# Kernel optimization log

Measured on AMD Instinct MI355X. Metric: run time of the kernel, lower is better.

## Reference

```python
import jax, jax.numpy as jnp
import numpy as np

K = 5
B = 3.0
MIN_BW = 1e-3
MIN_BH = 1e-3
MIN_D = 1e-3


def _mlp(x, w0, b0, w1, b1):
    # Linear -> Tanh -> Linear (hidden_dim=[512])
    return jnp.tanh(x @ w0 + b0) @ w1 + b1


def _unconstrained_rqs(x, Wu, Hu, Du):
    """Rational-quadratic spline (forward), identity outside [-B, B].
    x: [N, D2]; Wu/Hu: [N, D2, K]; Du: [N, D2, K-1].
    Note: faithful to the torch code, Wu/Hu arrive already softmaxed*2B and Du
    already softplused in NSF_CL.forward, then RQS re-normalizes them again."""
    inside = (x >= -B) & (x <= B)
    const = float(np.log(np.exp(1.0 - MIN_D) - 1.0))
    Dp = jnp.pad(Du, ((0, 0), (0, 0), (1, 1)), constant_values=const)  # [N,D2,K+1]

    widths = jax.nn.softmax(Wu, axis=-1)
    widths = MIN_BW + (1.0 - MIN_BW * K) * widths
    cw = jnp.pad(jnp.cumsum(widths, axis=-1), ((0, 0), (0, 0), (1, 0)))
    cw = 2.0 * B * cw - B
    cw = cw.at[..., 0].set(-B).at[..., -1].set(B)
    widths = cw[..., 1:] - cw[..., :-1]

    heights = jax.nn.softmax(Hu, axis=-1)
    heights = MIN_BH + (1.0 - MIN_BH * K) * heights
    ch = jnp.pad(jnp.cumsum(heights, axis=-1), ((0, 0), (0, 0), (1, 0)))
    ch = 2.0 * B * ch - B
    ch = ch.at[..., 0].set(-B).at[..., -1].set(B)
    heights = ch[..., 1:] - ch[..., :-1]

    deriv = MIN_D + jax.nn.softplus(Dp)  # [N,D2,K+1]

    xc = jnp.clip(x, -B, B)
    # bin search: index of bin containing xc
    idx = jnp.clip(jnp.sum((xc[..., None] >= cw).astype(jnp.int32), axis=-1) - 1, 0, K - 1)
    idx1 = idx[..., None]

    def g(a):
        return jnp.take_along_axis(a, idx1, axis=-1)[..., 0]

    in_cw = g(cw)
    in_w = g(widths)
    in_ch = g(ch)
    in_h = g(heights)
    delta = g(heights / widths)
    d_k = g(deriv)
    d_k1 = jnp.take_along_axis(deriv, idx1 + 1, axis=-1)[..., 0]

    theta = (xc - in_cw) / in_w
    t1m = theta * (1.0 - theta)
    numerator = in_h * (delta * theta * theta + d_k * t1m)
    denominator = delta + (d_k + d_k1 - 2.0 * delta) * t1m
    y = in_ch + numerator / denominator

    deriv_num = delta * delta * (d_k1 * theta * theta + 2.0 * delta * t1m + d_k * (1.0 - theta) ** 2)
    ld = jnp.log(deriv_num) - 2.0 * jnp.log(denominator)
    return jnp.where(inside, y, x), jnp.where(inside, ld, 0.0)


def _cond(out_flat, d2):
    out = out_flat.reshape(-1, d2, 3 * K - 1)
    Wu, Hu, Du = out[..., :K], out[..., K:2 * K], out[..., 2 * K:]
    Wu = 2.0 * B * jax.nn.softmax(Wu, axis=-1)
    Hu = 2.0 * B * jax.nn.softmax(Hu, axis=-1)
    Du = jax.nn.softplus(Du)
    return Wu, Hu, Du


def setup_inputs() -> dict:
    key = jax.random.key(0)
    ks = jax.random.split(key, 5)
    N, dim, hid = 32768, 256, 512
    half = dim // 2
    out_dim = half * (3 * K - 1)
    s0 = 1.0 / np.sqrt(half)
    s1 = 1.0 / np.sqrt(hid)
    return {
        "x": jax.random.normal(ks[0], (N, dim), dtype=jnp.float32),
        "f0_w0": jax.random.normal(ks[1], (half, hid), dtype=jnp.float32) * s0,
        "f0_b0": jnp.zeros((hid,), jnp.float32),
        "f0_w1": jax.random.normal(ks[2], (hid, out_dim), dtype=jnp.float32) * s1,
        "f0_b1": jnp.zeros((out_dim,), jnp.float32),
        "f1_w0": jax.random.normal(ks[3], (half, hid), dtype=jnp.float32) * s0,
        "f1_b0": jnp.zeros((hid,), jnp.float32),
        "f1_w1": jax.random.normal(ks[4], (hid, out_dim), dtype=jnp.float32) * s1,
        "f1_b1": jnp.zeros((out_dim,), jnp.float32),
    }


def reference(x, f0_w0, f0_b0, f0_w1, f0_b1, f1_w0, f1_b0, f1_w1, f1_b1):
    half = x.shape[1] // 2
    x0, x1 = x[:, :half], x[:, half:]
    Wu, Hu, Du = _cond(_mlp(x0, f0_w0, f0_b0, f0_w1, f0_b1), half)
    x1, ld1 = _unconstrained_rqs(x1, Wu, Hu, Du)
    Wu, Hu, Du = _cond(_mlp(x1, f1_w0, f1_b0, f1_w1, f1_b1), half)
    x0, ld0 = _unconstrained_rqs(x0, Wu, Hu, Du)
    z = jnp.concatenate([x0, x1], axis=1)
    log_det = jnp.sum(ld1, axis=1) + jnp.sum(ld0, axis=1)
    return z, log_det
```

## Files before the change

kernel.cpp:

```cpp
#include <hip/hip_runtime.h>
#include <math.h>


#define NROWS 32768
#define DIMX  256
#define HALF  128
#define HID   512
#define BM    64

typedef __attribute__((ext_vector_type(8))) short short8;
typedef __attribute__((ext_vector_type(4))) float f32x4;

__device__ __forceinline__ unsigned short f2bf(float x) {
    unsigned int u = __float_as_uint(x);
    u += 0x7fffu + ((u >> 16) & 1u);
    return (unsigned short)(u >> 16);
}

__device__ __forceinline__ float frcp(float x) { return __builtin_amdgcn_rcpf(x); }

__device__ __forceinline__ float spf(float x) {
    return fmaxf(x, 0.f) + __logf(1.f + __expf(-fabsf(x)));
}

__device__ __forceinline__ void dsm5(const float* P, float* out) {
    float e[5];
    float m = fmaxf(fmaxf(fmaxf(P[0], P[1]), fmaxf(P[2], P[3])), P[4]);
    float s = 0.f;
    #pragma unroll
    for (int p = 0; p < 5; ++p) { e[p] = __expf(P[p] - m); s += e[p]; }
    float r = 6.f * frcp(s);
    float s2 = 0.f;
    #pragma unroll
    for (int p = 0; p < 5; ++p) { e[p] = __expf(e[p] * r); s2 += e[p]; }
    float r2 = 0.995f * frcp(s2);
    #pragma unroll
    for (int p = 0; p < 5; ++p) out[p] = 1.0e-3f + e[p] * r2;
}

__device__ __forceinline__ void rqs_fast(const float* P, float xa, float& yo, float& ldo) {
    float wv[5], hv[5];
    dsm5(P, wv);
    dsm5(P + 5, hv);
    float dvi[4];
    #pragma unroll
    for (int p = 0; p < 4; ++p) dvi[p] = 1.0e-3f + spf(spf(P[10 + p]));
    float xc = fminf(fmaxf(xa, -3.f), 3.f);
    float csw = wv[0], csh = hv[0];
    float in_cw = -3.f, in_ch = -3.f;
    float in_w = 6.f * csw, in_h = 6.f * csh;
    float dk = 1.f, dk1 = dvi[0];
    #pragma unroll
    for (int p = 1; p < 5; ++p) {
        float cwp = 6.f * csw - 3.f;
        float chp = 6.f * csh - 3.f;
        csw += wv[p]; csh += hv[p];
        float cwp1 = (p == 4) ? 3.f : (6.f * csw - 3.f);
        float chp1 = (p == 4) ? 3.f : (6.f * csh - 3.f);
        bool take = (xc >= cwp);
        in_cw = take ? cwp : in_cw;
        in_w  = take ? (cwp1 - cwp) : in_w;
        in_ch = take ? chp : in_ch;
        in_h  = take ? (chp1 - chp) : in_h;
        dk    = take ? dvi[p - 1] : dk;
        dk1   = take ? ((p == 4) ? 1.f : dvi[p]) : dk1;
    }
    float rw = frcp(in_w);
    float th = (xc - in_cw) * rw;
    float om = 1.f - th;
    float t1m = th * om;
    float delta = in_h * rw;
    float num = in_h * (delta * th * th + dk * t1m);
    float den = delta + (dk + dk1 - 2.f * delta) * t1m;
    float y = in_ch + num * frcp(den);
    float dnum = delta * delta * (dk1 * th * th + 2.f * delta * t1m + dk * om * om);
    float ld = __logf(dnum) - 2.f * __logf(den);
    bool inside = (xa >= -3.f) && (xa <= 3.f);
    yo  = inside ? y : xa;
    ldo = inside ? ld : 0.f;
}

__global__ void prep(const float* __restrict__ w1a, const float* __restrict__ w1b,
                     const float* __restrict__ w0a, const float* __restrict__ w0b,
                     const float* __restrict__ b1a, const float* __restrict__ b1b,
                     short* __restrict__ w1f, short* __restrict__ w0f, float* __restrict__ b1p) {
    int idx = blockIdx.x * 256 + threadIdx.x;
    if (idx < 262144) {
        int stage = idx >> 17, rem = idx & 131071;
        int d = rem >> 10, c2 = (rem >> 6) & 15, l = rem & 63;
        const float* src = stage ? w1b : w1a;
        int p = l & 15, g = l >> 4;
        short8 o;
        #pragma unroll
        for (int e = 0; e < 8; ++e) {
            int k = 32 * c2 + 8 * g + e;
            float v = (p < 14) ? src[(size_t)k * 1792 + d * 14 + p] : 0.f;
            o[e] = (short)f2bf(v);
        }
        *reinterpret_cast<short8*>(w1f + (size_t)stage * 1048576 + (size_t)rem * 8) = o;
    } else if (idx < 278528) {
        int r = idx - 262144;
        int stage = r >> 13, rem = r & 8191;
        int l = rem & 63;
        const float* src = stage ? w0b : w0a;
        int p = l & 15, g = l >> 4;
        int ct = rem >> 8, c = (rem >> 6) & 3;
        short8 o;
        #pragma unroll
        for (int e = 0; e < 8; ++e) {
            int k = 32 * c + 8 * g + e;
            o[e] = (short)f2bf(src[k * 512 + ct * 16 + p]);
        }
        *reinterpret_cast<short8*>(w0f + stage * 65536 + rem * 8) = o;
    } else if (idx < 282624) {
        int r = idx - 278528;
        int stage = r >> 11, rem = r & 2047;
        int d = rem >> 4, p = rem & 15;
        const float* src = stage ? b1b : b1a;
        b1p[stage * 2048 + rem] = (p < 14) ? src[d * 14 + p] : 0.f;
    }
}

template <int STAGE>
__global__ __launch_bounds__(256, 2)
void nsf_stage(const float* __restrict__ xin, float* __restrict__ zout,
               float* __restrict__ ld_out,
               const short* __restrict__ w0f, const float* __restrict__ b0,
               const short* __restrict__ w1f, const float* __restrict__ b1p) {
    __shared__ __align__(16) short hA2[32768];
    __shared__ __align__(16) float pbuf[4096];
    short* A1 = reinterpret_cast<short*>(pbuf);

    const int tid = threadIdx.x;
    const int lane = tid & 63;
    const int w = tid >> 6;
    const int n0 = blockIdx.x * BM;

    const float* cond = STAGE ? zout : xin;
    const int coff = STAGE ? HALF : 0;
    const int aoff = STAGE ? 0 : HALF;
    const int yoff = STAGE ? 0 : HALF;

    #pragma unroll
    for (int t = 0; t < 4; ++t) {
        int idx = t * 256 + tid;
        int fr = idx >> 6, l = idx & 63;
        int rt = fr >> 2, c = fr & 3;
        int row = rt * 16 + (l & 15);
        int kb = 32 * c + 8 * (l >> 4);
        const float* sp = cond + (size_t)(n0 + row) * DIMX + coff + kb;
        short8 o;
        #pragma unroll
        for (int e = 0; e < 8; ++e) o[e] = (short)f2bf(sp[e]);
        *reinterpret_cast<short8*>(A1 + idx * 8) = o;
    }
    __syncthreads();

    for (int rt = 0; rt < 4; ++rt) {
        short8 a1[4];
        #pragma unroll
        for (int c = 0; c < 4; ++c)
            a1[c] = *reinterpret_cast<const short8*>(A1 + ((rt * 4 + c) * 64 + lane) * 8);
        #pragma unroll
        for (int j = 0; j < 8; ++j) {
            int ct = w * 8 + j;
            f32x4 acc = {0.f, 0.f, 0.f, 0.f};
            #pragma unroll
            for (int c = 0; c < 4; ++c) {
                short8 b = *reinterpret_cast<const short8*>(w0f + ((ct * 4 + c) * 64 + lane) * 8);
                acc = __builtin_amdgcn_mfma_f32_16x16x32_bf16(a1[c], b, acc, 0, 0, 0);
            }
            float bv = b0[ct * 16 + (lane & 15)];
            int q = (2 * ct + ((lane & 15) >> 3)) & 3;
            int c2 = ct >> 1;
            #pragma unroll
            for (int r = 0; r < 4; ++r) {
                float av = acc[r] + bv;
                float e2 = __expf(2.f * av);
                float hvf = 1.f - 2.f * frcp(e2 + 1.f);
                int i = (lane >> 4) * 4 + r;
                hA2[((rt * 16 + c2) * 64 + (i + 16 * q)) * 8 + (lane & 7)] = (short)f2bf(hvf);
            }
        }
    }
    __syncthreads();

    float ldp[4] = {0.f, 0.f, 0.f, 0.f};
    float* pb = pbuf + w * 1024;
    for (int pr = 0; pr < 2; ++pr) {
        short8 a2[2][16];
        #pragma unroll
        for (int q = 0; q < 2; ++q)
            #pragma unroll
            for (int c2 = 0; c2 < 16; ++c2)
                a2[q][c2] = *reinterpret_cast<const short8*>(
                    hA2 + (((pr * 2 + q) * 16 + c2) * 64 + lane) * 8);
        for (int dg = 0; dg < 8; ++dg) {
            const int d0 = w * 32 + dg * 4;
            f32x4 acc[2][4];
            #pragma unroll
            for (int q = 0; q < 2; ++q)
                #pragma unroll
                for (int dd = 0; dd < 4; ++dd) acc[q][dd] = (f32x4){0.f, 0.f, 0.f, 0.f};
            #pragma unroll
            for (int c2 = 0; c2 < 16; ++c2) {
                #pragma unroll
                for (int dd = 0; dd < 4; ++dd) {
                    short8 b = *reinterpret_cast<const short8*>(
                        w1f + ((size_t)((d0 + dd) * 16 + c2) * 64 + lane) * 8);
                    acc[0][dd] = __builtin_amdgcn_mfma_f32_16x16x32_bf16(a2[0][c2], b, acc[0][dd], 0, 0, 0);
                    acc[1][dd] = __builtin_amdgcn_mfma_f32_16x16x32_bf16(a2[1][c2], b, acc[1][dd], 0, 0, 0);
                }
            }
            float bvv[4];
            #pragma unroll
            for (int dd = 0; dd < 4; ++dd) bvv[dd] = b1p[(d0 + dd) * 16 + (lane & 15)];
            #pragma unroll
            for (int q = 0; q < 2; ++q) {
                const int rt2 = pr * 2 + q;
                #pragma unroll
                for (int dd = 0; dd < 4; ++dd) {
                    #pragma unroll
                    for (int r = 0; r < 4; ++r) {
                        int rl = (lane >> 4) * 4 + r;
                        pb[dd * 256 + rl * 16 + ((lane & 15) ^ (((rl >> 1) & 3) << 2))] =
                            acc[q][dd][r] + bvv[dd];
                    }
                }
                asm volatile("s_waitcnt lgkmcnt(0)" ::: "memory");
                __builtin_amdgcn_sched_barrier(0);
                {
                    int rl = lane & 15, dd = lane >> 4;
                    int s = ((rl >> 1) & 3) << 2;
                    const float* rb = pb + dd * 256 + rl * 16;
                    float P[16];
                    #pragma unroll
                    for (int qd = 0; qd < 4; ++qd) {
                        f32x4 v = *reinterpret_cast<const f32x4*>(rb + ((qd * 4) ^ s));
                        P[qd * 4 + 0] = v[0]; P[qd * 4 + 1] = v[1];
                        P[qd * 4 + 2] = v[2]; P[qd * 4 + 3] = v[3];
                    }
                    size_t nrow = (size_t)(n0 + rt2 * 16 + rl) * DIMX;
                    float xa = xin[nrow + aoff + d0 + dd];
                    float y, ldv;
                    rqs_fast(P, xa, y, ldv);
                    zout[nrow + yoff + d0 + dd] = y;
                    ldv += __shfl_xor(ldv, 16, 64);
                    ldv += __shfl_xor(ldv, 32, 64);
                    ldp[rt2] += ldv;
                }
            }
        }
    }

    if (lane < 16) {
        #pragma unroll
        for (int rt2 = 0; rt2 < 4; ++rt2) pb[rt2 * 16 + lane] = ldp[rt2];
    }
    __syncthreads();
    if (tid < BM) {
        float s = pbuf[tid] + pbuf[1024 + tid] + pbuf[2048 + tid] + pbuf[3072 + tid];
        if (STAGE == 0) ld_out[n0 + tid] = s;
        else            ld_out[n0 + tid] += s;
    }
}

extern "C" void kernel_launch(void* const* d_in, const int* in_sizes, int n_in,
                              void* d_out, int out_size, void* d_ws, size_t ws_size,
                              hipStream_t stream) {
    const float* x     = (const float*)d_in[0];
    const float* f0_w0 = (const float*)d_in[1];
    const float* f0_b0 = (const float*)d_in[2];
    const float* f0_w1 = (const float*)d_in[3];
    const float* f0_b1 = (const float*)d_in[4];
    const float* f1_w0 = (const float*)d_in[5];
    const float* f1_b0 = (const float*)d_in[6];
    const float* f1_w1 = (const float*)d_in[7];
    const float* f1_b1 = (const float*)d_in[8];

    float* zout = (float*)d_out;
    float* ld   = zout + (size_t)NROWS * DIMX;

    short* w1f = (short*)d_ws;
    short* w0f = (short*)((char*)d_ws + 4 * 1024 * 1024);
    float* b1p = (float*)((char*)d_ws + 4 * 1024 * 1024 + 256 * 1024);

    prep<<<1104, 256, 0, stream>>>(f0_w1, f1_w1, f0_w0, f1_w0, f0_b1, f1_b1, w1f, w0f, b1p);
    nsf_stage<0><<<NROWS / BM, 256, 0, stream>>>(x, zout, ld, w0f, f0_b0, w1f, b1p);
    nsf_stage<1><<<NROWS / BM, 256, 0, stream>>>(x, zout, ld, w0f + 65536, f1_b0,
                                                 w1f + 1048576, b1p + 2048);
}
```

Measured before the change: 399.6 us.

## Halve row tile to 32 with 8 waves per block and reorder W1 layout

Reduces the per-block row tile from 64 to 32 rows while doubling threads to 512 (8 waves), each wave handling 16 output dims instead of 32. The second GEMM no longer preloads all hidden A fragments into registers; it streams them from LDS per k-chunk, and the prepacked W1 layout is reordered so k-chunk is the outer index. This aims to cut register pressure and raise occupancy (launch bounds 512,4), at the cost of more LDS reads and twice the W1 reuse traffic per row.

Result: slower. 696.9 us (+74.4%).

```diff
diff --git a/kernel.cpp b/kernel.cpp
--- a/kernel.cpp
+++ b/kernel.cpp
@@ -6,7 +6,7 @@
 #define DIMX  256
 #define HALF  128
 #define HID   512
-#define BM    64
+#define BM    32
 
 typedef __attribute__((ext_vector_type(8))) short short8;
 typedef __attribute__((ext_vector_type(4))) float f32x4;
@@ -87,7 +87,7 @@
     int idx = blockIdx.x * 256 + threadIdx.x;
     if (idx < 262144) {
         int stage = idx >> 17, rem = idx & 131071;
-        int d = rem >> 10, c2 = (rem >> 6) & 15, l = rem & 63;
+        int c2 = rem >> 13, d = (rem >> 6) & 127, l = rem & 63;
         const float* src = stage ? w1b : w1a;
         int p = l & 15, g = l >> 4;
         short8 o;
@@ -122,13 +122,13 @@
 }
 
 template <int STAGE>
-__global__ __launch_bounds__(256, 2)
+__global__ __launch_bounds__(512, 4)
 void nsf_stage(const float* __restrict__ xin, float* __restrict__ zout,
                float* __restrict__ ld_out,
                const short* __restrict__ w0f, const float* __restrict__ b0,
                const short* __restrict__ w1f, const float* __restrict__ b1p) {
-    __shared__ __align__(16) short hA2[32768];
-    __shared__ __align__(16) float pbuf[4096];
+    __shared__ __align__(16) short hA2[16384];
+    __shared__ __align__(16) float pbuf[8192];
     short* A1 = reinterpret_cast<short*>(pbuf);
 
     const int tid = threadIdx.x;
@@ -141,10 +141,8 @@
     const int aoff = STAGE ? 0 : HALF;
     const int yoff = STAGE ? 0 : HALF;
 
-    #pragma unroll
-    for (int t = 0; t < 4; ++t) {
-        int idx = t * 256 + tid;
-        int fr = idx >> 6, l = idx & 63;
+    {
+        int fr = tid >> 6, l = tid & 63;
         int rt = fr >> 2, c = fr & 3;
         int row = rt * 16 + (l & 15);
         int kb = 32 * c + 8 * (l >> 4);
@@ -152,18 +150,18 @@
         short8 o;
         #pragma unroll
         for (int e = 0; e < 8; ++e) o[e] = (short)f2bf(sp[e]);
-        *reinterpret_cast<short8*>(A1 + idx * 8) = o;
+        *reinterpret_cast<short8*>(A1 + tid * 8) = o;
     }
     __syncthreads();
 
-    for (int rt = 0; rt < 4; ++rt) {
+    for (int rt = 0; rt < 2; ++rt) {
         short8 a1[4];
         #pragma unroll
         for (int c = 0; c < 4; ++c)
             a1[c] = *reinterpret_cast<const short8*>(A1 + ((rt * 4 + c) * 64 + lane) * 8);
         #pragma unroll
-        for (int j = 0; j < 8; ++j) {
-            int ct = w * 8 + j;
+        for (int j = 0; j < 4; ++j) {
+            int ct = w * 4 + j;
             f32x4 acc = {0.f, 0.f, 0.f, 0.f};
             #pragma unroll
             for (int c = 0; c < 4; ++c) {
@@ -185,81 +183,75 @@
     }
     __syncthreads();
 
-    float ldp[4] = {0.f, 0.f, 0.f, 0.f};
+    float ldp[2] = {0.f, 0.f};
     float* pb = pbuf + w * 1024;
-    for (int pr = 0; pr < 2; ++pr) {
-        short8 a2[2][16];
+    for (int dg = 0; dg < 4; ++dg) {
+        const int d0 = w * 16 + dg * 4;
+        f32x4 acc[2][4];
         #pragma unroll
         for (int q = 0; q < 2; ++q)
             #pragma unroll
-            for (int c2 = 0; c2 < 16; ++c2)
-                a2[q][c2] = *reinterpret_cast<const short8*>(
-                    hA2 + (((pr * 2 + q) * 16 + c2) * 64 + lane) * 8);
-        for (int dg = 0; dg < 8; ++dg) {
-            const int d0 = w * 32 + dg * 4;
-            f32x4 acc[2][4];
-            #pragma unroll
-            for (int q = 0; q < 2; ++q)
+            for (int dd = 0; dd < 4; ++dd) acc[q][dd] = (f32x4){0.f, 0.f, 0.f, 0.f};
+        #pragma unroll
+        for (int c2 = 0; c2 < 16; ++c2) {
+            short8 a20 = *reinterpret_cast<const short8*>(hA2 + (c2 * 64 + lane) * 8);
+            short8 a21 = *reinterpret_cast<const short8*>(hA2 + ((16 + c2) * 64 + lane) * 8);
+            #pragma unroll
+            for (int dd = 0; dd < 4; ++dd) {
+                short8 b = *reinterpret_cast<const short8*>(
+                    w1f + ((size_t)(c2 * 128 + d0 + dd) * 64 + lane) * 8);
+                acc[0][dd] = __builtin_amdgcn_mfma_f32_16x16x32_bf16(a20, b, acc[0][dd], 0, 0, 0);
+                acc[1][dd] = __builtin_amdgcn_mfma_f32_16x16x32_bf16(a21, b, acc[1][dd], 0, 0, 0);
+            }
+        }
+        float bvv[4];
+        #pragma unroll
+        for (int dd = 0; dd < 4; ++dd) bvv[dd] = b1p[(d0 + dd) * 16 + (lane & 15)];
+        #pragma unroll
+        for (int rt2 = 0; rt2 < 2; ++rt2) {
+            #pragma unroll
+            for (int dd = 0; dd < 4; ++dd) {
                 #pragma unroll
-                for (int dd = 0; dd < 4; ++dd) acc[q][dd] = (f32x4){0.f, 0.f, 0.f, 0.f};
-            #pragma unroll
-            for (int c2 = 0; c2 < 16; ++c2) {
+                for (int r = 0; r < 4; ++r) {
+                    int rl = (lane >> 4) * 4 + r;
+                    pb[dd * 256 + rl * 16 + ((lane & 15) ^ (((rl >> 1) & 3) << 2))] =
+                        acc[rt2][dd][r] + bvv[dd];
+                }
+            }
+            asm volatile("s_waitcnt lgkmcnt(0)" ::: "memory");
+            __builtin_amdgcn_sched_barrier(0);
+            {
+                int rl = lane & 15, dd = lane >> 4;
+                int s = ((rl >> 1) & 3) << 2;
+                const float* rb = pb + dd * 256 + rl * 16;
+                float P[16];
                 #pragma unroll
-                for (int dd = 0; dd < 4; ++dd) {
-                    short8 b = *reinterpret_cast<const short8*>(
-                        w1f + ((size_t)((d0 + dd) * 16 + c2) * 64 + lane) * 8);
-                    acc[0][dd] = __builtin_amdgcn_mfma_f32_16x16x32_bf16(a2[0][c2], b, acc[0][dd], 0, 0, 0);
-                    acc[1][dd] = __builtin_amdgcn_mfma_f32_16x16x32_bf16(a2[1][c2], b, acc[1][dd], 0, 0, 0);
+                for (int qd = 0; qd < 4; ++qd) {
+                    f32x4 v = *reinterpret_cast<const f32x4*>(rb + ((qd * 4) ^ s));
+                    P[qd * 4 + 0] = v[0]; P[qd * 4 + 1] = v[1];
+                    P[qd * 4 + 2] = v[2]; P[qd * 4 + 3] = v[3];
                 }
-            }
-            float bvv[4];
-            #pragma unroll
-            for (int dd = 0; dd < 4; ++dd) bvv[dd] = b1p[(d0 + dd) * 16 + (lane & 15)];
-            #pragma unroll
-            for (int q = 0; q < 2; ++q) {
-                const int rt2 = pr * 2 + q;
-                #pragma unroll
-                for (int dd = 0; dd < 4; ++dd) {
-                    #pragma unroll
-                    for (int r = 0; r < 4; ++r) {
-                        int rl = (lane >> 4) * 4 + r;
-                        pb[dd * 256 + rl * 16 + ((lane & 15) ^ (((rl >> 1) & 3) << 2))] =
-                            acc[q][dd][r] + bvv[dd];
-                    }
-                }
-                asm volatile("s_waitcnt lgkmcnt(0)" ::: "memory");
-                __builtin_amdgcn_sched_barrier(0);
-                {
-                    int rl = lane & 15, dd = lane >> 4;
-                    int s = ((rl >> 1) & 3) << 2;
-                    const float* rb = pb + dd * 256 + rl * 16;
-                    float P[16];
-                    #pragma unroll
-                    for (int qd = 0; qd < 4; ++qd) {
-                        f32x4 v = *reinterpret_cast<const f32x4*>(rb + ((qd * 4) ^ s));
-                        P[qd * 4 + 0] = v[0]; P[qd * 4 + 1] = v[1];
-                        P[qd * 4 + 2] = v[2]; P[qd * 4 + 3] = v[3];
-                    }
-                    size_t nrow = (size_t)(n0 + rt2 * 16 + rl) * DIMX;
-                    float xa = xin[nrow + aoff + d0 + dd];
-                    float y, ldv;
-                    rqs_fast(P, xa, y, ldv);
-                    zout[nrow + yoff + d0 + dd] = y;
-                    ldv += __shfl_xor(ldv, 16, 64);
-                    ldv += __shfl_xor(ldv, 32, 64);
-                    ldp[rt2] += ldv;
-                }
+                size_t nrow = (size_t)(n0 + rt2 * 16 + rl) * DIMX;
+                float xa = xin[nrow + aoff + d0 + dd];
+                float y, ldv;
+                rqs_fast(P, xa, y, ldv);
+                zout[nrow + yoff + d0 + dd] = y;
+                ldv += __shfl_xor(ldv, 16, 64);
+                ldv += __shfl_xor(ldv, 32, 64);
+                ldp[rt2] += ldv;
             }
         }
     }
 
     if (lane < 16) {
-        #pragma unroll
-        for (int rt2 = 0; rt2 < 4; ++rt2) pb[rt2 * 16 + lane] = ldp[rt2];
+        pb[lane] = ldp[0];
+        pb[16 + lane] = ldp[1];
     }
     __syncthreads();
     if (tid < BM) {
-        float s = pbuf[tid] + pbuf[1024 + tid] + pbuf[2048 + tid] + pbuf[3072 + tid];
+        float s = 0.f;
+        #pragma unroll
+        for (int ww = 0; ww < 8; ++ww) s += pbuf[ww * 1024 + tid];
         if (STAGE == 0) ld_out[n0 + tid] = s;
         else            ld_out[n0 + tid] += s;
     }
@@ -286,7 +278,7 @@
     float* b1p = (float*)((char*)d_ws + 4 * 1024 * 1024 + 256 * 1024);
 
     prep<<<1104, 256, 0, stream>>>(f0_w1, f1_w1, f0_w0, f1_w0, f0_b1, f1_b1, w1f, w0f, b1p);
-    nsf_stage<0><<<NROWS / BM, 256, 0, stream>>>(x, zout, ld, w0f, f0_b0, w1f, b1p);
-    nsf_stage<1><<<NROWS / BM, 256, 0, stream>>>(x, zout, ld, w0f + 65536, f1_b0,
+    nsf_stage<0><<<NROWS / BM, 512, 0, stream>>>(x, zout, ld, w0f, f0_b0, w1f, b1p);
+    nsf_stage<1><<<NROWS / BM, 512, 0, stream>>>(x, zout, ld, w0f + 65536, f1_b0,
                                                  w1f + 1048576, b1p + 2048);
 }
```

## Restructure second GEMM as transposed per-parameter MFMA tiles with folded bias

Applied to the files above, without the earlier changes.

Reorganizes the second MLP layer so the weights become the A operand. Each of the 14 spline parameters gets its own 16-dim MFMA tile, which removes the 16-wide padding (only 14 of 16 columns were useful) and the LDS round-trip used to gather parameters per thread. The bias is folded into the GEMM as an extra K chunk multiplied by a ones vector. Softmax is turned directly into cumulative sums. The row tile drops to 32 and occupancy rises to 4 blocks per CU. In exchange, weights are re-read from global/L2 per 32 rows instead of per 64, doubling weight traffic, and register pressure may be high.

Measured after the change: 1.350 ms. +237.8%, slower.

```diff
diff --git a/kernel.cpp b/kernel.cpp
--- a/kernel.cpp
+++ b/kernel.cpp
@@ -6,7 +6,7 @@
 #define DIMX  256
 #define HALF  128
 #define HID   512
-#define BM    64
+#define BM    32
 
 typedef __attribute__((ext_vector_type(8))) short short8;
 typedef __attribute__((ext_vector_type(4))) float f32x4;
@@ -23,7 +23,7 @@
     return fmaxf(x, 0.f) + __logf(1.f + __expf(-fabsf(x)));
 }
 
-__device__ __forceinline__ void dsm5(const float* P, float* out) {
+__device__ __forceinline__ void dsm5_cs(const float* P, float* cs) {
     float e[5];
     float m = fmaxf(fmaxf(fmaxf(P[0], P[1]), fmaxf(P[2], P[3])), P[4]);
     float s = 0.f;
@@ -34,29 +34,23 @@
     #pragma unroll
     for (int p = 0; p < 5; ++p) { e[p] = __expf(e[p] * r); s2 += e[p]; }
     float r2 = 0.995f * frcp(s2);
-    #pragma unroll
-    for (int p = 0; p < 5; ++p) out[p] = 1.0e-3f + e[p] * r2;
-}
-
-__device__ __forceinline__ void rqs_fast(const float* P, float xa, float& yo, float& ldo) {
-    float wv[5], hv[5];
-    dsm5(P, wv);
-    dsm5(P + 5, hv);
-    float dvi[4];
-    #pragma unroll
-    for (int p = 0; p < 4; ++p) dvi[p] = 1.0e-3f + spf(spf(P[10 + p]));
+    float run = 0.f;
+    #pragma unroll
+    for (int p = 0; p < 4; ++p) { run += e[p]; cs[p] = (float)(p + 1) * 1.0e-3f + r2 * run; }
+}
+
+__device__ __forceinline__ void rqs_cs(const float* csw, const float* csh, const float* dvi,
+                                       float xa, float& yo, float& ldo) {
     float xc = fminf(fmaxf(xa, -3.f), 3.f);
-    float csw = wv[0], csh = hv[0];
     float in_cw = -3.f, in_ch = -3.f;
-    float in_w = 6.f * csw, in_h = 6.f * csh;
+    float in_w = 6.f * csw[0], in_h = 6.f * csh[0];
     float dk = 1.f, dk1 = dvi[0];
     #pragma unroll
     for (int p = 1; p < 5; ++p) {
-        float cwp = 6.f * csw - 3.f;
-        float chp = 6.f * csh - 3.f;
-        csw += wv[p]; csh += hv[p];
-        float cwp1 = (p == 4) ? 3.f : (6.f * csw - 3.f);
-        float chp1 = (p == 4) ? 3.f : (6.f * csh - 3.f);
+        float cwp = 6.f * csw[p - 1] - 3.f;
+        float chp = 6.f * csh[p - 1] - 3.f;
+        float cwp1 = (p == 4) ? 3.f : (6.f * csw[p] - 3.f);
+        float chp1 = (p == 4) ? 3.f : (6.f * csh[p] - 3.f);
         bool take = (xc >= cwp);
         in_cw = take ? cwp : in_cw;
         in_w  = take ? (cwp1 - cwp) : in_w;
@@ -80,29 +74,43 @@
     ldo = inside ? ld : 0.f;
 }
 
+#define W1FRAGS 1904
+#define W1ELEMS (W1FRAGS * 64)
 __global__ void prep(const float* __restrict__ w1a, const float* __restrict__ w1b,
                      const float* __restrict__ w0a, const float* __restrict__ w0b,
                      const float* __restrict__ b1a, const float* __restrict__ b1b,
-                     short* __restrict__ w1f, short* __restrict__ w0f, float* __restrict__ b1p) {
+                     short* __restrict__ w1f, short* __restrict__ w0f) {
     int idx = blockIdx.x * 256 + threadIdx.x;
-    if (idx < 262144) {
-        int stage = idx >> 17, rem = idx & 131071;
-        int d = rem >> 10, c2 = (rem >> 6) & 15, l = rem & 63;
-        const float* src = stage ? w1b : w1a;
-        int p = l & 15, g = l >> 4;
+    if (idx < 2 * W1ELEMS) {
+        int s = idx / W1ELEMS;
+        int rem = idx - s * W1ELEMS;
+        int frag = rem >> 6, l = rem & 63;
+        int p = frag % 14;
+        int t = frag / 14;
+        int c2 = t % 17;
+        int dblk = t / 17;
+        const float* w1s = s ? w1b : w1a;
+        const float* b1s = s ? b1b : b1a;
+        int col = (dblk * 16 + (l & 15)) * 14 + p;
+        int g = l >> 4;
         short8 o;
         #pragma unroll
         for (int e = 0; e < 8; ++e) {
-            int k = 32 * c2 + 8 * g + e;
-            float v = (p < 14) ? src[(size_t)k * 1792 + d * 14 + p] : 0.f;
+            float v;
+            if (c2 < 16) {
+                int k = 32 * c2 + 8 * g + e;
+                v = w1s[(size_t)k * 1792 + col];
+            } else {
+                v = (g == 0 && e == 0) ? b1s[col] : 0.f;
+            }
             o[e] = (short)f2bf(v);
         }
-        *reinterpret_cast<short8*>(w1f + (size_t)stage * 1048576 + (size_t)rem * 8) = o;
-    } else if (idx < 278528) {
-        int r = idx - 262144;
-        int stage = r >> 13, rem = r & 8191;
+        *reinterpret_cast<short8*>(w1f + ((size_t)s * W1ELEMS + rem) * 8) = o;
+    } else if (idx < 2 * W1ELEMS + 16384) {
+        int r = idx - 2 * W1ELEMS;
+        int s = r >> 13, rem = r & 8191;
         int l = rem & 63;
-        const float* src = stage ? w0b : w0a;
+        const float* src = s ? w0b : w0a;
         int p = l & 15, g = l >> 4;
         int ct = rem >> 8, c = (rem >> 6) & 3;
         short8 o;
@@ -111,25 +119,19 @@
             int k = 32 * c + 8 * g + e;
             o[e] = (short)f2bf(src[k * 512 + ct * 16 + p]);
         }
-        *reinterpret_cast<short8*>(w0f + stage * 65536 + rem * 8) = o;
-    } else if (idx < 282624) {
-        int r = idx - 278528;
-        int stage = r >> 11, rem = r & 2047;
-        int d = rem >> 4, p = rem & 15;
-        const float* src = stage ? b1b : b1a;
-        b1p[stage * 2048 + rem] = (p < 14) ? src[d * 14 + p] : 0.f;
+        *reinterpret_cast<short8*>(w0f + s * 65536 + rem * 8) = o;
     }
 }
 
 template <int STAGE>
-__global__ __launch_bounds__(256, 2)
+__global__ __launch_bounds__(256, 4)
 void nsf_stage(const float* __restrict__ xin, float* __restrict__ zout,
                float* __restrict__ ld_out,
                const short* __restrict__ w0f, const float* __restrict__ b0,
-               const short* __restrict__ w1f, const float* __restrict__ b1p) {
-    __shared__ __align__(16) short hA2[32768];
-    __shared__ __align__(16) float pbuf[4096];
-    short* A1 = reinterpret_cast<short*>(pbuf);
+               const short* __restrict__ w1f) {
+    __shared__ __align__(16) short hA2[16384];
+    __shared__ __align__(16) float aux[2048];
+    short* A1 = reinterpret_cast<short*>(aux);
 
     const int tid = threadIdx.x;
     const int lane = tid & 63;
@@ -142,7 +144,7 @@
     const int yoff = STAGE ? 0 : HALF;
 
     #pragma unroll
-    for (int t = 0; t < 4; ++t) {
+    for (int t = 0; t < 2; ++t) {
         int idx = t * 256 + tid;
         int fr = idx >> 6, l = idx & 63;
         int rt = fr >> 2, c = fr & 3;
@@ -156,7 +158,7 @@
     }
     __syncthreads();
 
-    for (int rt = 0; rt < 4; ++rt) {
+    for (int rt = 0; rt < 2; ++rt) {
         short8 a1[4];
         #pragma unroll
         for (int c = 0; c < 4; ++c)
@@ -185,81 +187,125 @@
     }
     __syncthreads();
 
-    float ldp[4] = {0.f, 0.f, 0.f, 0.f};
-    float* pb = pbuf + w * 1024;
-    for (int pr = 0; pr < 2; ++pr) {
-        short8 a2[2][16];
-        #pragma unroll
-        for (int q = 0; q < 2; ++q)
-            #pragma unroll
-            for (int c2 = 0; c2 < 16; ++c2)
-                a2[q][c2] = *reinterpret_cast<const short8*>(
-                    hA2 + (((pr * 2 + q) * 16 + c2) * 64 + lane) * 8);
-        for (int dg = 0; dg < 8; ++dg) {
-            const int d0 = w * 32 + dg * 4;
+    float ldacc[2] = {0.f, 0.f};
+    short8 vone = {0, 0, 0, 0, 0, 0, 0, 0};
+    if (lane < 16) vone[0] = (short)0x3F80;
+
+    for (int db = 0; db < 2; ++db) {
+        const int dblk = w * 2 + db;
+        const short* wbase = w1f + (size_t)dblk * 17 * 14 * 512;
+        float csW[2][4][4], csH[2][4][4], dvi[2][4][4];
+
+        {
+            f32x4 acc[2][5];
+            #pragma unroll
+            for (int q = 0; q < 2; ++q)
+                #pragma unroll
+                for (int p = 0; p < 5; ++p) acc[q][p] = (f32x4){0.f, 0.f, 0.f, 0.f};
+            for (int c2 = 0; c2 < 17; ++c2) {
+                short8 hb0 = (c2 < 16) ? *reinterpret_cast<const short8*>(hA2 + (c2 * 64 + lane) * 8) : vone;
+                short8 hb1 = (c2 < 16) ? *reinterpret_cast<const short8*>(hA2 + ((16 + c2) * 64 + lane) * 8) : vone;
+                const short* fb = wbase + (size_t)c2 * 14 * 512 + lane * 8;
+                #pragma unroll
+                for (int p = 0; p < 5; ++p) {
+                    short8 af = *reinterpret_cast<const short8*>(fb + p * 512);
+                    acc[0][p] = __builtin_amdgcn_mfma_f32_16x16x32_bf16(af, hb0, acc[0][p], 0, 0, 0);
+                    acc[1][p] = __builtin_amdgcn_mfma_f32_16x16x32_bf16(af, hb1, acc[1][p], 0, 0, 0);
+                }
+            }
+            #pragma unroll
+            for (int q = 0; q < 2; ++q)
+                #pragma unroll
+                for (int r = 0; r < 4; ++r) {
+                    float P[5] = {acc[q][0][r], acc[q][1][r], acc[q][2][r], acc[q][3][r], acc[q][4][r]};
+                    float cs[4];
+                    dsm5_cs(P, cs);
+                    #pragma unroll
+                    for (int i = 0; i < 4; ++i) csW[q][i][r] = cs[i];
+                }
+        }
+        {
+            f32x4 acc[2][5];
+            #pragma unroll
+            for (int q = 0; q < 2; ++q)
+                #pragma unroll
+                for (int p = 0; p < 5; ++p) acc[q][p] = (f32x4){0.f, 0.f, 0.f, 0.f};
+            for (int c2 = 0; c2 < 17; ++c2) {
+                short8 hb0 = (c2 < 16) ? *reinterpret_cast<const short8*>(hA2 + (c2 * 64 + lane) * 8) : vone;
+                short8 hb1 = (c2 < 16) ? *reinterpret_cast<const short8*>(hA2 + ((16 + c2) * 64 + lane) * 8) : vone;
+                const short* fb = wbase + (size_t)c2 * 14 * 512 + lane * 8;
+                #pragma unroll
+                for (int p = 0; p < 5; ++p) {
+                    short8 af = *reinterpret_cast<const short8*>(fb + (5 + p) * 512);
+                    acc[0][p] = __builtin_amdgcn_mfma_f32_16x16x32_bf16(af, hb0, acc[0][p], 0, 0, 0);
+                    acc[1][p] = __builtin_amdgcn_mfma_f32_16x16x32_bf16(af, hb1, acc[1][p], 0, 0, 0);
+                }
+            }
+            #pragma unroll
+            for (int q = 0; q < 2; ++q)
+                #pragma unroll
+                for (int r = 0; r < 4; ++r) {
+                    float P[5] = {acc[q][0][r], acc[q][1][r], acc[q][2][r], acc[q][3][r], acc[q][4][r]};
+                    float cs[4];
+                    dsm5_cs(P, cs);
+                    #pragma unroll
+                    for (int i = 0; i < 4; ++i) csH[q][i][r] = cs[i];
+                }
+        }
+        {
             f32x4 acc[2][4];
             #pragma unroll
             for (int q = 0; q < 2; ++q)
                 #pragma unroll
-                for (int dd = 0; dd < 4; ++dd) acc[q][dd] = (f32x4){0.f, 0.f, 0.f, 0.f};
-            #pragma unroll
-            for (int c2 = 0; c2 < 16; ++c2) {
-                #pragma unroll
-                for (int dd = 0; dd < 4; ++dd) {
-                    short8 b = *reinterpret_cast<const short8*>(
-                        w1f + ((size_t)((d0 + dd) * 16 + c2) * 64 + lane) * 8);
-                    acc[0][dd] = __builtin_amdgcn_mfma_f32_16x16x32_bf16(a2[0][c2], b, acc[0][dd], 0, 0, 0);
-                    acc[1][dd] = __builtin_amdgcn_mfma_f32_16x16x32_bf16(a2[1][c2], b, acc[1][dd], 0, 0, 0);
-                }
-            }
-            float bvv[4];
-            #pragma unroll
-            for (int dd = 0; dd < 4; ++dd) bvv[dd] = b1p[(d0 + dd) * 16 + (lane & 15)];
-            #pragma unroll
-            for (int q = 0; q < 2; ++q) {
-                const int rt2 = pr * 2 + q;
-                #pragma unroll
-                for (int dd = 0; dd < 4; ++dd) {
+                for (int p = 0; p < 4; ++p) acc[q][p] = (f32x4){0.f, 0.f, 0.f, 0.f};
+            for (int c2 = 0; c2 < 17; ++c2) {
+                short8 hb0 = (c2 < 16) ? *reinterpret_cast<const short8*>(hA2 + (c2 * 64 + lane) * 8) : vone;
+                short8 hb1 = (c2 < 16) ? *reinterpret_cast<const short8*>(hA2 + ((16 + c2) * 64 + lane) * 8) : vone;
+                const short* fb = wbase + (size_t)c2 * 14 * 512 + lane * 8;
+                #pragma unroll
+                for (int p = 0; p < 4; ++p) {
+                    short8 af = *reinterpret_cast<const short8*>(fb + (10 + p) * 512);
+                    acc[0][p] = __builtin_amdgcn_mfma_f32_16x16x32_bf16(af, hb0, acc[0][p], 0, 0, 0);
+                    acc[1][p] = __builtin_amdgcn_mfma_f32_16x16x32_bf16(af, hb1, acc[1][p], 0, 0, 0);
+                }
+            }
+            #pragma unroll
+            for (int q = 0; q < 2; ++q)
+                #pragma unroll
+                for (int r = 0; r < 4; ++r)
                     #pragma unroll
-                    for (int r = 0; r < 4; ++r) {
-                        int rl = (lane >> 4) * 4 + r;
-                        pb[dd * 256 + rl * 16 + ((lane & 15) ^ (((rl >> 1) & 3) << 2))] =
-                            acc[q][dd][r] + bvv[dd];
-                    }
-                }
-                asm volatile("s_waitcnt lgkmcnt(0)" ::: "memory");
-                __builtin_amdgcn_sched_barrier(0);
-                {
-                    int rl = lane & 15, dd = lane >> 4;
-                    int s = ((rl >> 1) & 3) << 2;
-                    const float* rb = pb + dd * 256 + rl * 16;
-                    float P[16];
-                    #pragma unroll
-                    for (int qd = 0; qd < 4; ++qd) {
-                        f32x4 v = *reinterpret_cast<const f32x4*>(rb + ((qd * 4) ^ s));
-                        P[qd * 4 + 0] = v[0]; P[qd * 4 + 1] = v[1];
-                        P[qd * 4 + 2] = v[2]; P[qd * 4 + 3] = v[3];
-                    }
-                    size_t nrow = (size_t)(n0 + rt2 * 16 + rl) * DIMX;
-                    float xa = xin[nrow + aoff + d0 + dd];
-                    float y, ldv;
-                    rqs_fast(P, xa, y, ldv);
-                    zout[nrow + yoff + d0 + dd] = y;
-                    ldv += __shfl_xor(ldv, 16, 64);
-                    ldv += __shfl_xor(ldv, 32, 64);
-                    ldp[rt2] += ldv;
-                }
-            }
-        }
-    }
-
+                    for (int p = 0; p < 4; ++p)
+                        dvi[q][p][r] = 1.0e-3f + spf(spf(acc[q][p][r]));
+        }
+        #pragma unroll
+        for (int q = 0; q < 2; ++q) {
+            #pragma unroll
+            for (int r = 0; r < 4; ++r) {
+                float cw_[4] = {csW[q][0][r], csW[q][1][r], csW[q][2][r], csW[q][3][r]};
+                float ch_[4] = {csH[q][0][r], csH[q][1][r], csH[q][2][r], csH[q][3][r]};
+                float dv_[4] = {dvi[q][0][r], dvi[q][1][r], dvi[q][2][r], dvi[q][3][r]};
+                int n = n0 + q * 16 + (lane & 15);
+                int d = dblk * 16 + (lane >> 4) * 4 + r;
+                float xa = xin[(size_t)n * DIMX + aoff + d];
+                float y, ldv;
+                rqs_cs(cw_, ch_, dv_, xa, y, ldv);
+                zout[(size_t)n * DIMX + yoff + d] = y;
+                ldacc[q] += ldv;
+            }
+        }
+    }
+
+    float s0 = ldacc[0], s1 = ldacc[1];
+    s0 += __shfl_xor(s0, 16, 64); s0 += __shfl_xor(s0, 32, 64);
+    s1 += __shfl_xor(s1, 16, 64); s1 += __shfl_xor(s1, 32, 64);
+    __syncthreads();
     if (lane < 16) {
-        #pragma unroll
-        for (int rt2 = 0; rt2 < 4; ++rt2) pb[rt2 * 16 + lane] = ldp[rt2];
+        aux[w * 32 + lane] = s0;
+        aux[w * 32 + 16 + lane] = s1;
     }
     __syncthreads();
     if (tid < BM) {
-        float s = pbuf[tid] + pbuf[1024 + tid] + pbuf[2048 + tid] + pbuf[3072 + tid];
+        float s = aux[tid] + aux[32 + tid] + aux[64 + tid] + aux[96 + tid];
         if (STAGE == 0) ld_out[n0 + tid] = s;
         else            ld_out[n0 + tid] += s;
     }
@@ -282,11 +328,10 @@
     float* ld   = zout + (size_t)NROWS * DIMX;
 
     short* w1f = (short*)d_ws;
-    short* w0f = (short*)((char*)d_ws + 4 * 1024 * 1024);
-    float* b1p = (float*)((char*)d_ws + 4 * 1024 * 1024 + 256 * 1024);
-
-    prep<<<1104, 256, 0, stream>>>(f0_w1, f1_w1, f0_w0, f1_w0, f0_b1, f1_b1, w1f, w0f, b1p);
-    nsf_stage<0><<<NROWS / BM, 256, 0, stream>>>(x, zout, ld, w0f, f0_b0, w1f, b1p);
+    short* w0f = (short*)((char*)d_ws + (size_t)2 * W1ELEMS * 16);
+
+    prep<<<1016, 256, 0, stream>>>(f0_w1, f1_w1, f0_w0, f1_w0, f0_b1, f1_b1, w1f, w0f);
+    nsf_stage<0><<<NROWS / BM, 256, 0, stream>>>(x, zout, ld, w0f, f0_b0, w1f);
     nsf_stage<1><<<NROWS / BM, 256, 0, stream>>>(x, zout, ld, w0f + 65536, f1_b0,
-                                                 w1f + 1048576, b1p + 2048);
-}
+                                                 w1f + (size_t)W1ELEMS * 8);
+}
```
